# Performance work log

Measured on AMD Instinct MI355X. Metric: run time of the kernel, lower is better.

## Reference

```python
import jax, jax.numpy as jnp
import numpy as np
import math

EMBED = 512
DIM2 = 768

def setup_inputs() -> dict:
    key = jax.random.key(0)
    ks = jax.random.split(key, 14)
    B, L1, L2 = 16, 2048, 1024
    s1 = 1.0 / math.sqrt(EMBED)
    s2 = 1.0 / math.sqrt(DIM2)
    inp = {
        'input_tensor1': jax.random.normal(ks[0], (B, EMBED, L1), jnp.float32),
        'input_tensor2': jax.random.normal(ks[1], (B, DIM2, L2), jnp.float32),
        # Linear params for modality 1 (512 -> 512)
        'Wq1': jax.random.normal(ks[2], (EMBED, EMBED), jnp.float32) * s1,
        'bq1': jnp.zeros((EMBED,), jnp.float32),
        'Wk1': jax.random.normal(ks[3], (EMBED, EMBED), jnp.float32) * s1,
        'bk1': jnp.zeros((EMBED,), jnp.float32),
        'Wv1': jax.random.normal(ks[4], (EMBED, EMBED), jnp.float32) * s1,
        'bv1': jnp.zeros((EMBED,), jnp.float32),
        # Linear params for modality 2 (768 -> 512)
        'Wq2': jax.random.normal(ks[5], (DIM2, EMBED), jnp.float32) * s2,
        'bq2': jnp.zeros((EMBED,), jnp.float32),
        'Wk2': jax.random.normal(ks[6], (DIM2, EMBED), jnp.float32) * s2,
        'bk2': jnp.zeros((EMBED,), jnp.float32),
        'Wv2': jax.random.normal(ks[7], (DIM2, EMBED), jnp.float32) * s2,
        'bv2': jnp.zeros((EMBED,), jnp.float32),
    }
    return inp


def reference(input_tensor1, input_tensor2,
              Wq1, bq1, Wk1, bk1, Wv1, bv1,
              Wq2, bq2, Wk2, bk2, Wv2, bv2):
    scale = 1.0 / math.sqrt(EMBED)
    # [B, C, L] -> [B, L, C]
    x1 = jnp.swapaxes(input_tensor1, 1, 2)  # [B, L1, 512]
    x2 = jnp.swapaxes(input_tensor2, 1, 2)  # [B, L2, 768]
    q1 = x1 @ Wq1 + bq1  # [B, L1, E]
    k1 = x1 @ Wk1 + bk1
    v1 = x1 @ Wv1 + bv1
    q2 = x2 @ Wq2 + bq2  # [B, L2, E]
    k2 = x2 @ Wk2 + bk2
    v2 = x2 @ Wv2 + bv2
    # direction 1: queries from modality 2 attend to modality 1
    scores1 = jnp.einsum('bif,bjf->bij', q2, k1) * scale  # [B, L2, L1]
    probs1 = jax.nn.sigmoid(scores1)
    ctx1 = jnp.einsum('bij,bjf->bif', probs1, v1)  # [B, L2, E]
    # direction 2: queries from modality 1 attend to modality 2
    scores2 = jnp.einsum('bif,bjf->bij', q1, k2) * scale  # [B, L1, L2]
    probs2 = jax.nn.sigmoid(scores2)
    ctx2 = jnp.einsum('bij,bjf->bif', probs2, v2)  # [B, L1, E]
    return (ctx2, probs2, ctx1, probs1)
```

## Files before the change

### kernel.cpp

```cpp
#include <hip/hip_runtime.h>
#include <hip/hip_bf16.h>

#define DEVFN __device__ __forceinline__

typedef __attribute__((ext_vector_type(4))) float f32x4;
typedef __attribute__((ext_vector_type(8))) short s16x8;
typedef __attribute__((ext_vector_type(2))) short s16x2;
typedef __attribute__((ext_vector_type(8))) __bf16 bf16x8;

union FragU { s16x8 s; bf16x8 b; };

DEVFN short f2bs(float x) {
  union { __hip_bfloat16 h; short s; } u;
  u.h = __float2bfloat16(x);
  return u.s;
}

DEVFN void gload16(const void* g, void* l) {
  __builtin_amdgcn_global_load_lds(
      (const __attribute__((address_space(1))) void*)g,
      (__attribute__((address_space(3))) void*)l, 16, 0, 0);
}

template <int N> DEVFN void waitcnt_vm() {
  if constexpr (N == 0) asm volatile("s_waitcnt vmcnt(0)" ::: "memory");
  else if constexpr (N == 3) asm volatile("s_waitcnt vmcnt(3)" ::: "memory");
  else if constexpr (N == 4) asm volatile("s_waitcnt vmcnt(4)" ::: "memory");
  else if constexpr (N == 6) asm volatile("s_waitcnt vmcnt(6)" ::: "memory");
  else if constexpr (N == 8) asm volatile("s_waitcnt vmcnt(8)" ::: "memory");
  else static_assert(N == 0, "unsupported vmcnt");
}

__global__ __launch_bounds__(256) void transpose_cvt(
    const float* __restrict__ in, short* __restrict__ out, int C, int L) {
  __shared__ float tile[64][33];
  const int l0 = blockIdx.x * 32, c0 = blockIdx.y * 64;
  const size_t base = (size_t)blockIdx.z * C * L;
  const int tx = threadIdx.x, ty = threadIdx.y;
#pragma unroll
  for (int i = ty; i < 64; i += 8)
    tile[i][tx] = in[base + (size_t)(c0 + i) * L + l0 + tx];
  __syncthreads();
#pragma unroll
  for (int i = ty; i < 32; i += 8) {
    s16x2 v;
    v[0] = f2bs(tile[2 * tx][i]);
    v[1] = f2bs(tile[2 * tx + 1][i]);
    *(s16x2*)&out[base + (size_t)(l0 + i) * C + c0 + 2 * tx] = v;
  }
}

__global__ __launch_bounds__(256) void prep_weights(
    const float* __restrict__ Wq1, const float* __restrict__ Wk1,
    const float* __restrict__ Wv1, const float* __restrict__ Wq2,
    const float* __restrict__ Wk2, const float* __restrict__ Wv2,
    short* wq1t, short* wk1t, short* wv1t,
    short* wq2t, short* wk2t, short* wv2t,
    const float* __restrict__ bq1, const float* __restrict__ bk1,
    const float* __restrict__ bq2, const float* __restrict__ bk2,
    float* b1c, float* b2c) {
  const int z = blockIdx.z;
  if (z == 6) {
    if (blockIdx.y != 0 || blockIdx.x >= 8) return;
    const int bx = blockIdx.x;
    const int tid = threadIdx.y * 32 + threadIdx.x;
    const int i = (bx & 3) * 256 + tid;
    const float* s = (bx < 4) ? ((i < 512) ? bq1 : bk1)
                              : ((i < 512) ? bq2 : bk2);
    float* d = (bx < 4) ? b1c : b2c;
    d[i] = s[i & 511];
    return;
  }
  const float* W; short* O; int C;
  switch (z) {
    case 0: W = Wq1; O = wq1t; C = 512; break;
    case 1: W = Wk1; O = wk1t; C = 512; break;
    case 2: W = Wv1; O = wv1t; C = 512; break;
    case 3: W = Wq2; O = wq2t; C = 768; break;
    case 4: W = Wk2; O = wk2t; C = 768; break;
    default: W = Wv2; O = wv2t; C = 768; break;
  }
  if (blockIdx.y * 64 >= (unsigned)C) return;
  const int L = 512;
  __shared__ float tile[64][33];
  const int l0 = blockIdx.x * 32, c0 = blockIdx.y * 64;
  const int tx = threadIdx.x, ty = threadIdx.y;
#pragma unroll
  for (int i = ty; i < 64; i += 8)
    tile[i][tx] = W[(size_t)(c0 + i) * L + l0 + tx];
  __syncthreads();
#pragma unroll
  for (int i = ty; i < 32; i += 8) {
    s16x2 v;
    v[0] = f2bs(tile[2 * tx][i]);
    v[1] = f2bs(tile[2 * tx + 1][i]);
    *(s16x2*)&O[(size_t)(l0 + i) * C + c0 + 2 * tx] = v;
  }
}

template <int OUTMODE, int BIASMODE, int MR>
__global__ __launch_bounds__(512, 2) void gemm8(
    const short* __restrict__ Ap, const short* __restrict__ Btp,
    const float* __restrict__ bias, void* __restrict__ Cptr,
    short* __restrict__ C2p,
    int K, int lda, int ldb, int ldc,
    long long sA, long long sB, long long sC, float scale) {
  constexpr int BM = MR * 32;
  constexpr int BN = 256;
  constexpr int LA = BM / 128;
  constexpr int LB = BN / 128;
  constexpr int LPT = LA + LB;
  constexpr int ABYTES = BM * 64;
  constexpr int BUFB = (BM + BN) * 64;
  constexpr int MH = MR / 2;
  __shared__ __align__(16) char smem[4 * BUFB];
  const int tid = threadIdx.x;
  const int lane = tid & 63, wid = tid >> 6;
  const int wm = wid >> 2, wn = wid & 3;

  const unsigned gx = gridDim.x, gy = gridDim.y, gz = gridDim.z;
  const unsigned NB = gx * gy * gz;
  unsigned h = blockIdx.x + gx * (blockIdx.y + gy * blockIdx.z);
  unsigned l = ((NB & 7u) == 0u) ? (h & 7u) * (NB >> 3) + (h >> 3) : h;
  const unsigned bx = l % gx;
  const unsigned rem = l / gx;
  const unsigned by = rem % gy;
  const unsigned bz = rem / gy;

  const int zb = bz;
  const int m0 = by * BM, n0 = bx * BN;
  const char* Ab = (const char*)(Ap + (size_t)zb * sA);
  const char* Bb = (const char*)(Btp + (size_t)zb * sB);
  const size_t lda2 = (size_t)lda * 2, ldb2 = (size_t)ldb * 2;

  int s_r[2], s_cb[2];
#pragma unroll
  for (int j = 0; j < 2; ++j) {
    const int d = j * 8192 + tid * 16;
    const int line = d >> 7;
    s_r[j] = line * 2 + ((d >> 6) & 1);
    s_cb[j] = (d & 63) ^ ((line & 3) << 4);
  }

  f32x4 acc[MR][4] = {};
  const int frow = lane & 15, fkg = lane >> 4;

  int ra[MR], rb[4];
#pragma unroll
  for (int mf = 0; mf < MR; ++mf) {
    const int R = wm * (MR * 16) + mf * 16 + frow;
    ra[mf] = (R >> 1) * 128 + (R & 1) * 64 + ((fkg * 16) ^ (((R >> 1) & 3) << 4));
  }
#pragma unroll
  for (int nf = 0; nf < 4; ++nf) {
    const int R = wn * 64 + nf * 16 + frow;
    rb[nf] = (R >> 1) * 128 + (R & 1) * 64 + ((fkg * 16) ^ (((R >> 1) & 3) << 4));
  }

  const int NT = K >> 5;

#define STAGE_A(t)                                                       \
  {                                                                      \
    char* base_ = smem + ((t) & 3) * BUFB;                               \
    const size_t kb_ = (size_t)(t) * 64;                                 \
    _Pragma("unroll")                                                    \
    for (int j = 0; j < LA; ++j)                                         \
      gload16(Ab + (size_t)(m0 + s_r[j]) * lda2 + kb_ + s_cb[j],         \
              base_ + j * 8192 + tid * 16);                              \
  }
#define STAGE_B(t)                                                       \
  {                                                                      \
    char* base_ = smem + ((t) & 3) * BUFB + ABYTES;                      \
    const size_t kb_ = (size_t)(t) * 64;                                 \
    _Pragma("unroll")                                                    \
    for (int j = 0; j < LB; ++j)                                         \
      gload16(Bb + (size_t)(n0 + s_r[j]) * ldb2 + kb_ + s_cb[j],         \
              base_ + j * 8192 + tid * 16);                              \
  }

  STAGE_A(0); STAGE_B(0);
  STAGE_A(1); STAGE_B(1);
  STAGE_A(2); STAGE_B(2);
  waitcnt_vm<2 * LPT>();
  __builtin_amdgcn_sched_barrier(0);
  __builtin_amdgcn_s_barrier();
  __builtin_amdgcn_sched_barrier(0);

  for (int t = 0; t < NT; ++t) {
    const char* la = smem + (t & 3) * BUFB;
    const char* lb = la + ABYTES;
    FragU fa[MR], fb[4];
    if (t + 3 < NT) STAGE_A(t + 3);
#pragma unroll
    for (int mf = 0; mf < MH; ++mf) fa[mf].s = *(const s16x8*)(la + ra[mf]);
#pragma unroll
    for (int nf = 0; nf < 4; ++nf) fb[nf].s = *(const s16x8*)(lb + rb[nf]);
    __builtin_amdgcn_s_barrier();
    asm volatile("s_waitcnt lgkmcnt(0)" ::: "memory");
    __builtin_amdgcn_sched_barrier(0);
    __builtin_amdgcn_s_setprio(1);
#pragma unroll
    for (int mf = 0; mf < MH; ++mf)
#pragma unroll
      for (int nf = 0; nf < 4; ++nf)
        acc[mf][nf] = __builtin_amdgcn_mfma_f32_16x16x32_bf16(
            fa[mf].b, fb[nf].b, acc[mf][nf], 0, 0, 0);
    __builtin_amdgcn_s_setprio(0);
    __builtin_amdgcn_s_barrier();
    if (t + 3 < NT) STAGE_B(t + 3);
#pragma unroll
    for (int mf = MH; mf < MR; ++mf) fa[mf].s = *(const s16x8*)(la + ra[mf]);
    __builtin_amdgcn_s_barrier();
    asm volatile("s_waitcnt lgkmcnt(0)" ::: "memory");
    __builtin_amdgcn_sched_barrier(0);
    __builtin_amdgcn_s_setprio(1);
#pragma unroll
    for (int mf = MH; mf < MR; ++mf)
#pragma unroll
      for (int nf = 0; nf < 4; ++nf)
        acc[mf][nf] = __builtin_amdgcn_mfma_f32_16x16x32_bf16(
            fa[mf].b, fb[nf].b, acc[mf][nf], 0, 0, 0);
    __builtin_amdgcn_s_setprio(0);
    if (t + 3 < NT) {
      waitcnt_vm<2 * LPT>();
    } else if (t + 2 < NT) {
      waitcnt_vm<LPT>();
    } else if (t + 1 < NT) {
      waitcnt_vm<0>();
    } else {
      break;
    }
    __builtin_amdgcn_sched_barrier(0);
    __builtin_amdgcn_s_barrier();
    __builtin_amdgcn_sched_barrier(0);
  }
#undef STAGE_A
#undef STAGE_B

  const int rbase = (lane >> 4) * 4, cbase = lane & 15;
#pragma unroll
  for (int mf = 0; mf < MR; ++mf) {
#pragma unroll
    for (int nf = 0; nf < 4; ++nf) {
      const int gcol = n0 + wn * 64 + nf * 16 + cbase;
      float bn = (BIASMODE == 1) ? bias[gcol] : 0.f;
#pragma unroll
      for (int r = 0; r < 4; ++r) {
        const int grow = m0 + wm * (MR * 16) + mf * 16 + rbase + r;
        const size_t idx = (size_t)zb * sC + (size_t)grow * ldc + gcol;
        float v = acc[mf][nf][r];
        if constexpr (BIASMODE == 2) v += bias[grow]; else v += bn;
        if constexpr (OUTMODE == 0) {
          ((short*)Cptr)[idx] = f2bs(v);
        } else if constexpr (OUTMODE == 1) {
          ((float*)Cptr)[idx] = v;
        } else if constexpr (OUTMODE == 2) {
          ((float*)Cptr)[idx] = 1.0f / (1.0f + __expf(-v * scale));
        } else {
          float p = 1.0f / (1.0f + __expf(-v * scale));
          ((float*)Cptr)[idx] = p;
          C2p[idx] = f2bs(p);
        }
      }
    }
  }
}

template <int OUTMODE, int BIASMODE, int AF32>
__global__ __launch_bounds__(256) void gemm_bt(
    const void* __restrict__ Aptr, const short* __restrict__ Btp,
    const float* __restrict__ bias, void* __restrict__ Cptr,
    short* __restrict__ C2p,
    int K, int lda, int ldb, int ldc,
    long long sA, long long sB, long long sC, float scale) {
  __shared__ __align__(16) short lsA[128 * 64];
  __shared__ __align__(16) short lsB[128 * 64];
  const int tid = threadIdx.x;
  const int lane = tid & 63, wid = tid >> 6;
  const int zb = blockIdx.z;
  const int m0 = blockIdx.y * 128, n0 = blockIdx.x * 128;
  const short* Ab = AF32 ? nullptr : (const short*)Aptr + (size_t)zb * sA;
  const float* Af = AF32 ? (const float*)Aptr + (size_t)zb * sA : nullptr;
  const short* Bt = Btp + (size_t)zb * sB;

  f32x4 acc[4][4] = {};
  const int woffM = (wid >> 1) * 64, woffN = (wid & 1) * 64;
  const int frow = lane & 15, fkg = lane >> 4;

  for (int k0 = 0; k0 < K; k0 += 64) {
    if (k0) __syncthreads();
    if constexpr (!AF32) {
#pragma unroll
      for (int i = 0; i < 4; ++i) {
        const int f = i * 4096 + tid * 16;
        const int row = f >> 7, colb = f & 127;
        gload16((const char*)Ab + ((size_t)(m0 + row) * lda + k0) * 2 + colb,
                (char*)lsA + f);
      }
    } else {
#pragma unroll
      for (int i = 0; i < 8; ++i) {
        int f = tid + i * 256;
        int row = f >> 4, c4 = f & 15;
        f32x4 v = *(const f32x4*)&Af[(size_t)(m0 + row) * lda + k0 + c4 * 4];
        union { short s[4]; unsigned long long q; } cv;
#pragma unroll
        for (int j = 0; j < 4; ++j) cv.s[j] = f2bs(v[j]);
        *(unsigned long long*)&lsA[row * 64 + c4 * 4] = cv.q;
      }
    }
#pragma unroll
    for (int i = 0; i < 4; ++i) {
      const int f = i * 4096 + tid * 16;
      const int row = f >> 7, colb = f & 127;
      gload16((const char*)Bt + ((size_t)(n0 + row) * ldb + k0) * 2 + colb,
              (char*)lsB + f);
    }
    __syncthreads();
#pragma unroll
    for (int kk = 0; kk < 2; ++kk) {
      const int kb = kk * 32 + fkg * 8;
      FragU fa[4], fb[4];
#pragma unroll
      for (int mf = 0; mf < 4; ++mf)
        fa[mf].s = *(const s16x8*)&lsA[(woffM + mf * 16 + frow) * 64 + kb];
#pragma unroll
      for (int nf = 0; nf < 4; ++nf)
        fb[nf].s = *(const s16x8*)&lsB[(woffN + nf * 16 + frow) * 64 + kb];
#pragma unroll
      for (int mf = 0; mf < 4; ++mf)
#pragma unroll
        for (int nf = 0; nf < 4; ++nf)
          acc[mf][nf] = __builtin_amdgcn_mfma_f32_16x16x32_bf16(
              fa[mf].b, fb[nf].b, acc[mf][nf], 0, 0, 0);
    }
  }

  const int rbase = (lane >> 4) * 4, cbase = lane & 15;
#pragma unroll
  for (int mf = 0; mf < 4; ++mf) {
#pragma unroll
    for (int nf = 0; nf < 4; ++nf) {
      const int gcol = n0 + woffN + nf * 16 + cbase;
      float bn = (BIASMODE == 1) ? bias[gcol] : 0.f;
#pragma unroll
      for (int r = 0; r < 4; ++r) {
        const int grow = m0 + woffM + mf * 16 + rbase + r;
        const size_t idx = (size_t)zb * sC + (size_t)grow * ldc + gcol;
        float v = acc[mf][nf][r];
        if constexpr (BIASMODE == 2) v += bias[grow]; else v += bn;
        if constexpr (OUTMODE == 0) {
          ((short*)Cptr)[idx] = f2bs(v);
        } else if constexpr (OUTMODE == 1) {
          ((float*)Cptr)[idx] = v;
        } else if constexpr (OUTMODE == 2) {
          ((float*)Cptr)[idx] = 1.0f / (1.0f + __expf(-v * scale));
        } else {
          float p = 1.0f / (1.0f + __expf(-v * scale));
          ((float*)Cptr)[idx] = p;
          C2p[idx] = f2bs(p);
        }
      }
    }
  }
}

extern "C" void kernel_launch(void* const* d_in, const int* in_sizes, int n_in,
                              void* d_out, int out_size, void* d_ws, size_t ws_size,
                              hipStream_t stream) {
  const float* in1 = (const float*)d_in[0];
  const float* in2 = (const float*)d_in[1];
  const float* Wq1 = (const float*)d_in[2];  const float* bq1 = (const float*)d_in[3];
  const float* Wk1 = (const float*)d_in[4];  const float* bk1 = (const float*)d_in[5];
  const float* Wv1 = (const float*)d_in[6];  const float* bv1 = (const float*)d_in[7];
  const float* Wq2 = (const float*)d_in[8];  const float* bq2 = (const float*)d_in[9];
  const float* Wk2 = (const float*)d_in[10]; const float* bk2 = (const float*)d_in[11];
  const float* Wv2 = (const float*)d_in[12]; const float* bv2 = (const float*)d_in[13];

  float* out = (float*)d_out;
  float* ctx2   = out;
  float* probs2 = out + (size_t)16 * 2048 * 512;
  float* ctx1   = probs2 + (size_t)16 * 2048 * 1024;
  float* probs1 = ctx1 + (size_t)16 * 1024 * 512;

  char* ws = (char*)d_ws;
  constexpr size_t O_WQ1T = 0;
  constexpr size_t O_WK1T = O_WQ1T + (size_t)512 * 512 * 2;
  constexpr size_t O_WV1T = O_WK1T + (size_t)512 * 512 * 2;
  constexpr size_t O_WQ2T = O_WV1T + (size_t)512 * 512 * 2;
  constexpr size_t O_WK2T = O_WQ2T + (size_t)768 * 512 * 2;
  constexpr size_t O_WV2T = O_WK2T + (size_t)768 * 512 * 2;
  constexpr size_t O_B1   = O_WV2T + (size_t)768 * 512 * 2;
  constexpr size_t O_B2   = O_B1 + 4096;
  constexpr size_t O_QK1  = O_B2 + 4096;
  constexpr size_t O_V1T  = O_QK1 + (size_t)32768 * 1024 * 2;
  constexpr size_t O_QK2  = O_V1T + (size_t)16 * 512 * 2048 * 2;
  constexpr size_t O_V2T  = O_QK2 + (size_t)16384 * 1024 * 2;
  constexpr size_t O_X1B  = O_V2T + (size_t)16 * 512 * 1024 * 2;
  constexpr size_t O_X2B  = O_X1B + (size_t)32768 * 512 * 2;
  constexpr size_t O_PB1  = O_X2B + (size_t)16384 * 768 * 2;
  constexpr size_t O_PB2  = O_PB1 + (size_t)16 * 1024 * 2048 * 2;
  constexpr size_t NEED_A = O_PB2 + (size_t)16 * 2048 * 1024 * 2;
  constexpr size_t NEED_B = O_PB1;

  short* wq1t = (short*)(ws + O_WQ1T);
  short* wk1t = (short*)(ws + O_WK1T);
  short* wv1t = (short*)(ws + O_WV1T);
  short* wq2t = (short*)(ws + O_WQ2T);
  short* wk2t = (short*)(ws + O_WK2T);
  short* wv2t = (short*)(ws + O_WV2T);
  float* b1c  = (float*)(ws + O_B1);
  float* b2c  = (float*)(ws + O_B2);
  short* qk1  = (short*)(ws + O_QK1);
  short* v1t  = (short*)(ws + O_V1T);
  short* qk2  = (short*)(ws + O_QK2);
  short* v2t  = (short*)(ws + O_V2T);
  short* x1b  = (short*)(ws + O_X1B);
  short* x2b  = (short*)(ws + O_X2B);
  short* pb1  = (short*)(ws + O_PB1);
  short* pb2  = (short*)(ws + O_PB2);

  const bool tierA = ws_size >= NEED_A;
  const bool tierB = ws_size >= NEED_B;
  if (!tierB) { x1b = (short*)probs1; x2b = (short*)probs2; }

  dim3 blk256(256), blk512(512);
  dim3 blkT(32, 8);

  transpose_cvt<<<dim3(64, 8, 16), blkT, 0, stream>>>(in1, x1b, 512, 2048);
  transpose_cvt<<<dim3(32, 12, 16), blkT, 0, stream>>>(in2, x2b, 768, 1024);
  prep_weights<<<dim3(16, 12, 7), blkT, 0, stream>>>(
      Wq1, Wk1, Wv1, Wq2, Wk2, Wv2, wq1t, wk1t, wv1t, wq2t, wk2t, wv2t,
      bq1, bk1, bq2, bk2, b1c, b2c);

  const float scale = 0.04419417382415922f;
  const short* q1p = qk1;
  const short* k1p = qk1 + 512;
  const short* q2p = qk2;
  const short* k2p = qk2 + 512;

  if (tierA) {
    gemm8<0, 1, 8><<<dim3(4, 128, 1), blk512, 0, stream>>>(
        x1b, wq1t, b1c, qk1, nullptr, 512, 512, 512, 1024, 0, 0, 0, 1.f);
    gemm8<0, 1, 8><<<dim3(4, 64, 1), blk512, 0, stream>>>(
        x2b, wq2t, b2c, qk2, nullptr, 768, 768, 768, 1024, 0, 0, 0, 1.f);
    gemm8<0, 2, 8><<<dim3(8, 2, 16), blk512, 0, stream>>>(
        wv1t, x1b, bv1, v1t, nullptr, 512, 512, 512, 2048,
        0, (long long)2048 * 512, (long long)512 * 2048, 1.f);
    gemm8<0, 2, 4><<<dim3(4, 4, 16), blk512, 0, stream>>>(
        wv2t, x2b, bv2, v2t, nullptr, 768, 768, 768, 1024,
        0, (long long)1024 * 768, (long long)512 * 1024, 1.f);
    gemm8<3, 0, 8><<<dim3(8, 4, 16), blk512, 0, stream>>>(
        q2p, k1p, nullptr, probs1, pb1, 512, 1024, 1024, 2048,
        (long long)1024 * 1024, (long long)2048 * 1024, (long long)1024 * 2048, scale);
    gemm8<3, 0, 8><<<dim3(4, 8, 16), blk512, 0, stream>>>(
        q1p, k2p, nullptr, probs2, pb2, 512, 1024, 1024, 1024,
        (long long)2048 * 1024, (long long)1024 * 1024, (long long)2048 * 1024, scale);
    gemm8<1, 0, 4><<<dim3(2, 8, 16), blk512, 0, stream>>>(
        pb1, v1t, nullptr, ctx1, nullptr, 2048, 2048, 2048, 512,
        (long long)1024 * 2048, (long long)512 * 2048, (long long)1024 * 512, 1.f);
    gemm8<1, 0, 8><<<dim3(2, 8, 16), blk512, 0, stream>>>(
        pb2, v2t, nullptr, ctx2, nullptr, 1024, 1024, 1024, 512,
        (long long)2048 * 1024, (long long)512 * 1024, (long long)2048 * 512, 1.f);
  } else {
    gemm_bt<0, 1, 0><<<dim3(8, 256, 1), blk256, 0, stream>>>(
        x1b, wq1t, b1c, qk1, nullptr, 512, 512, 512, 1024, 0, 0, 0, 1.f);
    gemm_bt<0, 1, 0><<<dim3(8, 128, 1), blk256, 0, stream>>>(
        x2b, wq2t, b2c, qk2, nullptr, 768, 768, 768, 1024, 0, 0, 0, 1.f);
    gemm_bt<0, 2, 0><<<dim3(16, 4, 16), blk256, 0, stream>>>(
        wv1t, x1b, bv1, v1t, nullptr, 512, 512, 512, 2048,
        0, (long long)2048 * 512, (long long)512 * 2048, 1.f);
    gemm_bt<0, 2, 0><<<dim3(8, 4, 16), blk256, 0, stream>>>(
        wv2t, x2b, bv2, v2t, nullptr, 768, 768, 768, 1024,
        0, (long long)1024 * 768, (long long)512 * 1024, 1.f);
    gemm_bt<2, 0, 0><<<dim3(16, 8, 16), blk256, 0, stream>>>(
        q2p, k1p, nullptr, probs1, nullptr, 512, 1024, 1024, 2048,
        (long long)1024 * 1024, (long long)2048 * 1024, (long long)1024 * 2048, scale);
    gemm_bt<2, 0, 0><<<dim3(8, 16, 16), blk256, 0, stream>>>(
        q1p, k2p, nullptr, probs2, nullptr, 512, 1024, 1024, 1024,
        (long long)2048 * 1024, (long long)1024 * 1024, (long long)2048 * 1024, scale);
    gemm_bt<1, 0, 1><<<dim3(4, 8, 16), blk256, 0, stream>>>(
        probs1, v1t, nullptr, ctx1, nullptr, 2048, 2048, 2048, 512,
        (long long)1024 * 2048, (long long)512 * 2048, (long long)1024 * 512, 1.f);
    gemm_bt<1, 0, 1><<<dim3(4, 16, 16), blk256, 0, stream>>>(
        probs2, v2t, nullptr, ctx2, nullptr, 1024, 1024, 1024, 512,
        (long long)2048 * 1024, (long long)512 * 1024, (long long)2048 * 512, 1.f);
  }
}
```

Baseline: 458.7 us.

## Replace 8-wave 256-wide GEMM with 4-wave 128-wide triple-buffered kernel

Swaps the 512-thread GEMM (BN=256, 4-stage buffer, split A/B staging with two MFMA phases per k-step) for a 256-thread kernel with BN=128. It uses 3 LDS buffers with a prefetch depth of 2 and a single fused stage/compute phase per k-step. Each wave still computes MW×4 fragments. Grids double in the N dimension. The aim is smaller LDS per block and fewer barriers, at the cost of less B reuse per block and a shallower prefetch pipeline, which may expose memory latency.

```diff
diff --git a/kernel.cpp b/kernel.cpp
--- a/kernel.cpp
+++ b/kernel.cpp
@@ -24,7 +24,6 @@
 
 template <int N> DEVFN void waitcnt_vm() {
   if constexpr (N == 0) asm volatile("s_waitcnt vmcnt(0)" ::: "memory");
-  else if constexpr (N == 3) asm volatile("s_waitcnt vmcnt(3)" ::: "memory");
   else if constexpr (N == 4) asm volatile("s_waitcnt vmcnt(4)" ::: "memory");
   else if constexpr (N == 6) asm volatile("s_waitcnt vmcnt(6)" ::: "memory");
   else if constexpr (N == 8) asm volatile("s_waitcnt vmcnt(8)" ::: "memory");
@@ -98,25 +97,23 @@
   }
 }
 
-template <int OUTMODE, int BIASMODE, int MR>
-__global__ __launch_bounds__(512, 2) void gemm8(
+template <int OUTMODE, int BIASMODE, int MW>
+__global__ __launch_bounds__(256, 2) void gemm4(
     const short* __restrict__ Ap, const short* __restrict__ Btp,
     const float* __restrict__ bias, void* __restrict__ Cptr,
     short* __restrict__ C2p,
     int K, int lda, int ldb, int ldc,
     long long sA, long long sB, long long sC, float scale) {
-  constexpr int BM = MR * 32;
-  constexpr int BN = 256;
-  constexpr int LA = BM / 128;
-  constexpr int LB = BN / 128;
+  constexpr int BM = MW * 32;
+  constexpr int LA = BM / 64;
+  constexpr int LB = 2;
   constexpr int LPT = LA + LB;
   constexpr int ABYTES = BM * 64;
-  constexpr int BUFB = (BM + BN) * 64;
-  constexpr int MH = MR / 2;
-  __shared__ __align__(16) char smem[4 * BUFB];
+  constexpr int BUFB = (BM + 128) * 64;
+  __shared__ __align__(16) char smem[3 * BUFB];
   const int tid = threadIdx.x;
   const int lane = tid & 63, wid = tid >> 6;
-  const int wm = wid >> 2, wn = wid & 3;
+  const int wm = wid >> 1, wn = wid & 1;
 
   const unsigned gx = gridDim.x, gy = gridDim.y, gz = gridDim.z;
   const unsigned NB = gx * gy * gz;
@@ -128,27 +125,27 @@
   const unsigned bz = rem / gy;
 
   const int zb = bz;
-  const int m0 = by * BM, n0 = bx * BN;
+  const int m0 = by * BM, n0 = bx * 128;
   const char* Ab = (const char*)(Ap + (size_t)zb * sA);
   const char* Bb = (const char*)(Btp + (size_t)zb * sB);
   const size_t lda2 = (size_t)lda * 2, ldb2 = (size_t)ldb * 2;
 
-  int s_r[2], s_cb[2];
-#pragma unroll
-  for (int j = 0; j < 2; ++j) {
-    const int d = j * 8192 + tid * 16;
+  int s_r[LA], s_cb[LA];
+#pragma unroll
+  for (int j = 0; j < LA; ++j) {
+    const int d = j * 4096 + tid * 16;
     const int line = d >> 7;
     s_r[j] = line * 2 + ((d >> 6) & 1);
     s_cb[j] = (d & 63) ^ ((line & 3) << 4);
   }
 
-  f32x4 acc[MR][4] = {};
+  f32x4 acc[MW][4] = {};
   const int frow = lane & 15, fkg = lane >> 4;
 
-  int ra[MR], rb[4];
-#pragma unroll
-  for (int mf = 0; mf < MR; ++mf) {
-    const int R = wm * (MR * 16) + mf * 16 + frow;
+  int ra[MW], rb[4];
+#pragma unroll
+  for (int mf = 0; mf < MW; ++mf) {
+    const int R = wm * (MW * 16) + mf * 16 + frow;
     ra[mf] = (R >> 1) * 128 + (R & 1) * 64 + ((fkg * 16) ^ (((R >> 1) & 3) << 4));
   }
 #pragma unroll
@@ -159,71 +156,47 @@
 
   const int NT = K >> 5;
 
-#define STAGE_A(t)                                                       \
+#define STAGE(t)                                                         \
   {                                                                      \
-    char* base_ = smem + ((t) & 3) * BUFB;                               \
+    char* base_ = smem + ((t) % 3) * BUFB;                               \
     const size_t kb_ = (size_t)(t) * 64;                                 \
     _Pragma("unroll")                                                    \
     for (int j = 0; j < LA; ++j)                                         \
       gload16(Ab + (size_t)(m0 + s_r[j]) * lda2 + kb_ + s_cb[j],         \
-              base_ + j * 8192 + tid * 16);                              \
-  }
-#define STAGE_B(t)                                                       \
-  {                                                                      \
-    char* base_ = smem + ((t) & 3) * BUFB + ABYTES;                      \
-    const size_t kb_ = (size_t)(t) * 64;                                 \
+              base_ + j * 4096 + tid * 16);                              \
     _Pragma("unroll")                                                    \
     for (int j = 0; j < LB; ++j)                                         \
       gload16(Bb + (size_t)(n0 + s_r[j]) * ldb2 + kb_ + s_cb[j],         \
-              base_ + j * 8192 + tid * 16);                              \
-  }
-
-  STAGE_A(0); STAGE_B(0);
-  STAGE_A(1); STAGE_B(1);
-  STAGE_A(2); STAGE_B(2);
-  waitcnt_vm<2 * LPT>();
+              base_ + ABYTES + j * 4096 + tid * 16);                     \
+  }
+
+  STAGE(0);
+  STAGE(1);
+  waitcnt_vm<LPT>();
   __builtin_amdgcn_sched_barrier(0);
   __builtin_amdgcn_s_barrier();
   __builtin_amdgcn_sched_barrier(0);
 
   for (int t = 0; t < NT; ++t) {
-    const char* la = smem + (t & 3) * BUFB;
+    if (t + 2 < NT) STAGE(t + 2);
+    const char* la = smem + (t % 3) * BUFB;
     const char* lb = la + ABYTES;
-    FragU fa[MR], fb[4];
-    if (t + 3 < NT) STAGE_A(t + 3);
-#pragma unroll
-    for (int mf = 0; mf < MH; ++mf) fa[mf].s = *(const s16x8*)(la + ra[mf]);
+    FragU fa[MW], fb[4];
+#pragma unroll
+    for (int mf = 0; mf < MW; ++mf) fa[mf].s = *(const s16x8*)(la + ra[mf]);
 #pragma unroll
     for (int nf = 0; nf < 4; ++nf) fb[nf].s = *(const s16x8*)(lb + rb[nf]);
-    __builtin_amdgcn_s_barrier();
     asm volatile("s_waitcnt lgkmcnt(0)" ::: "memory");
     __builtin_amdgcn_sched_barrier(0);
     __builtin_amdgcn_s_setprio(1);
 #pragma unroll
-    for (int mf = 0; mf < MH; ++mf)
+    for (int mf = 0; mf < MW; ++mf)
 #pragma unroll
       for (int nf = 0; nf < 4; ++nf)
         acc[mf][nf] = __builtin_amdgcn_mfma_f32_16x16x32_bf16(
             fa[mf].b, fb[nf].b, acc[mf][nf], 0, 0, 0);
     __builtin_amdgcn_s_setprio(0);
-    __builtin_amdgcn_s_barrier();
-    if (t + 3 < NT) STAGE_B(t + 3);
-#pragma unroll
-    for (int mf = MH; mf < MR; ++mf) fa[mf].s = *(const s16x8*)(la + ra[mf]);
-    __builtin_amdgcn_s_barrier();
-    asm volatile("s_waitcnt lgkmcnt(0)" ::: "memory");
-    __builtin_amdgcn_sched_barrier(0);
-    __builtin_amdgcn_s_setprio(1);
-#pragma unroll
-    for (int mf = MH; mf < MR; ++mf)
-#pragma unroll
-      for (int nf = 0; nf < 4; ++nf)
-        acc[mf][nf] = __builtin_amdgcn_mfma_f32_16x16x32_bf16(
-            fa[mf].b, fb[nf].b, acc[mf][nf], 0, 0, 0);
-    __builtin_amdgcn_s_setprio(0);
-    if (t + 3 < NT) {
-      waitcnt_vm<2 * LPT>();
-    } else if (t + 2 < NT) {
+    if (t + 2 < NT) {
       waitcnt_vm<LPT>();
     } else if (t + 1 < NT) {
       waitcnt_vm<0>();
@@ -234,19 +207,18 @@
     __builtin_amdgcn_s_barrier();
     __builtin_amdgcn_sched_barrier(0);
   }
-#undef STAGE_A
-#undef STAGE_B
+#undef STAGE
 
   const int rbase = (lane >> 4) * 4, cbase = lane & 15;
 #pragma unroll
-  for (int mf = 0; mf < MR; ++mf) {
+  for (int mf = 0; mf < MW; ++mf) {
 #pragma unroll
     for (int nf = 0; nf < 4; ++nf) {
       const int gcol = n0 + wn * 64 + nf * 16 + cbase;
       float bn = (BIASMODE == 1) ? bias[gcol] : 0.f;
 #pragma unroll
       for (int r = 0; r < 4; ++r) {
-        const int grow = m0 + wm * (MR * 16) + mf * 16 + rbase + r;
+        const int grow = m0 + wm * (MW * 16) + mf * 16 + rbase + r;
         const size_t idx = (size_t)zb * sC + (size_t)grow * ldc + gcol;
         float v = acc[mf][nf][r];
         if constexpr (BIASMODE == 2) v += bias[grow]; else v += bn;
@@ -424,7 +396,7 @@
   const bool tierB = ws_size >= NEED_B;
   if (!tierB) { x1b = (short*)probs1; x2b = (short*)probs2; }
 
-  dim3 blk256(256), blk512(512);
+  dim3 blk256(256);
   dim3 blkT(32, 8);
 
   transpose_cvt<<<dim3(64, 8, 16), blkT, 0, stream>>>(in1, x1b, 512, 2048);
@@ -440,26 +412,26 @@
   const short* k2p = qk2 + 512;
 
   if (tierA) {
-    gemm8<0, 1, 8><<<dim3(4, 128, 1), blk512, 0, stream>>>(
+    gemm4<0, 1, 8><<<dim3(8, 128, 1), blk256, 0, stream>>>(
         x1b, wq1t, b1c, qk1, nullptr, 512, 512, 512, 1024, 0, 0, 0, 1.f);
-    gemm8<0, 1, 8><<<dim3(4, 64, 1), blk512, 0, stream>>>(
+    gemm4<0, 1, 8><<<dim3(8, 64, 1), blk256, 0, stream>>>(
         x2b, wq2t, b2c, qk2, nullptr, 768, 768, 768, 1024, 0, 0, 0, 1.f);
-    gemm8<0, 2, 8><<<dim3(8, 2, 16), blk512, 0, stream>>>(
+    gemm4<0, 2, 8><<<dim3(16, 2, 16), blk256, 0, stream>>>(
         wv1t, x1b, bv1, v1t, nullptr, 512, 512, 512, 2048,
         0, (long long)2048 * 512, (long long)512 * 2048, 1.f);
-    gemm8<0, 2, 4><<<dim3(4, 4, 16), blk512, 0, stream>>>(
+    gemm4<0, 2, 4><<<dim3(8, 4, 16), blk256, 0, stream>>>(
         wv2t, x2b, bv2, v2t, nullptr, 768, 768, 768, 1024,
         0, (long long)1024 * 768, (long long)512 * 1024, 1.f);
-    gemm8<3, 0, 8><<<dim3(8, 4, 16), blk512, 0, stream>>>(
+    gemm4<3, 0, 8><<<dim3(16, 4, 16), blk256, 0, stream>>>(
         q2p, k1p, nullptr, probs1, pb1, 512, 1024, 1024, 2048,
         (long long)1024 * 1024, (long long)2048 * 1024, (long long)1024 * 2048, scale);
-    gemm8<3, 0, 8><<<dim3(4, 8, 16), blk512, 0, stream>>>(
+    gemm4<3, 0, 8><<<dim3(8, 8, 16), blk256, 0, stream>>>(
         q1p, k2p, nullptr, probs2, pb2, 512, 1024, 1024, 1024,
         (long long)2048 * 1024, (long long)1024 * 1024, (long long)2048 * 1024, scale);
-    gemm8<1, 0, 4><<<dim3(2, 8, 16), blk512, 0, stream>>>(
+    gemm4<1, 0, 4><<<dim3(4, 8, 16), blk256, 0, stream>>>(
         pb1, v1t, nullptr, ctx1, nullptr, 2048, 2048, 2048, 512,
         (long long)1024 * 2048, (long long)512 * 2048, (long long)1024 * 512, 1.f);
-    gemm8<1, 0, 8><<<dim3(2, 8, 16), blk512, 0, stream>>>(
+    gemm4<1, 0, 8><<<dim3(4, 8, 16), blk256, 0, stream>>>(
         pb2, v2t, nullptr, ctx2, nullptr, 1024, 1024, 1024, 512,
         (long long)2048 * 1024, (long long)512 * 1024, (long long)2048 * 512, 1.f);
   } else {
```

New measurement: 474.9 us. +3.5%, slower.

## Merge paired GEMM launches into dual-problem kernels and use nontemporal fp32 stores

Applied to the files above, without the earlier changes.

The gemm8 kernel becomes gemm8d, which takes two independent GEMM problems and splits a flat 1D grid between them by block index. The QK, V, score/sigmoid and context GEMM pairs each run as one launch. This cuts launch count and lets the two problems share the GPU instead of each leaving a partially filled tail wave. The fp32 output stores (probs and ctx) now use nontemporal hints so they do not pollute cache. The V2/ctx2 halves are forced to share one MR tile size, which changes their tiling and could cost some efficiency.

```diff
diff --git a/kernel.cpp b/kernel.cpp
--- a/kernel.cpp
+++ b/kernel.cpp
@@ -99,12 +99,20 @@
 }
 
 template <int OUTMODE, int BIASMODE, int MR>
-__global__ __launch_bounds__(512, 2) void gemm8(
-    const short* __restrict__ Ap, const short* __restrict__ Btp,
-    const float* __restrict__ bias, void* __restrict__ Cptr,
-    short* __restrict__ C2p,
-    int K, int lda, int ldb, int ldc,
-    long long sA, long long sB, long long sC, float scale) {
+__global__ __launch_bounds__(512, 2) void gemm8d(
+    const short* __restrict__ A0, const short* __restrict__ B0,
+    const float* __restrict__ bias0, void* __restrict__ C0,
+    short* __restrict__ D0,
+    int K0, int lda0, int ldb0, int ldc0,
+    long long sA0, long long sB0, long long sC0,
+    unsigned gx0, unsigned gy0, unsigned nb0,
+    const short* __restrict__ A1, const short* __restrict__ B1,
+    const float* __restrict__ bias1, void* __restrict__ C1,
+    short* __restrict__ D1,
+    int K1, int lda1, int ldb1, int ldc1,
+    long long sA1, long long sB1, long long sC1,
+    unsigned gx1, unsigned gy1,
+    float scale) {
   constexpr int BM = MR * 32;
   constexpr int BN = 256;
   constexpr int LA = BM / 128;
@@ -118,10 +126,26 @@
   const int lane = tid & 63, wid = tid >> 6;
   const int wm = wid >> 2, wn = wid & 3;
 
-  const unsigned gx = gridDim.x, gy = gridDim.y, gz = gridDim.z;
-  const unsigned NB = gx * gy * gz;
-  unsigned h = blockIdx.x + gx * (blockIdx.y + gy * blockIdx.z);
-  unsigned l = ((NB & 7u) == 0u) ? (h & 7u) * (NB >> 3) + (h >> 3) : h;
+  const unsigned h = blockIdx.x;
+  const bool sec = h >= nb0;
+  const unsigned hh = sec ? h - nb0 : h;
+  const unsigned nb = sec ? gridDim.x - nb0 : nb0;
+  const unsigned gx = sec ? gx1 : gx0;
+  const unsigned gy = sec ? gy1 : gy0;
+  const short* Ap = sec ? A1 : A0;
+  const short* Btp = sec ? B1 : B0;
+  const float* bias = sec ? bias1 : bias0;
+  void* Cptr = sec ? C1 : C0;
+  short* C2p = sec ? D1 : D0;
+  const int K = sec ? K1 : K0;
+  const int lda = sec ? lda1 : lda0;
+  const int ldb = sec ? ldb1 : ldb0;
+  const int ldc = sec ? ldc1 : ldc0;
+  const long long sA = sec ? sA1 : sA0;
+  const long long sB = sec ? sB1 : sB0;
+  const long long sC = sec ? sC1 : sC0;
+
+  unsigned l = ((nb & 7u) == 0u) ? (hh & 7u) * (nb >> 3) + (hh >> 3) : hh;
   const unsigned bx = l % gx;
   const unsigned rem = l / gx;
   const unsigned by = rem % gy;
@@ -253,12 +277,13 @@
         if constexpr (OUTMODE == 0) {
           ((short*)Cptr)[idx] = f2bs(v);
         } else if constexpr (OUTMODE == 1) {
-          ((float*)Cptr)[idx] = v;
+          __builtin_nontemporal_store(v, &((float*)Cptr)[idx]);
         } else if constexpr (OUTMODE == 2) {
-          ((float*)Cptr)[idx] = 1.0f / (1.0f + __expf(-v * scale));
+          float p = 1.0f / (1.0f + __expf(-v * scale));
+          __builtin_nontemporal_store(p, &((float*)Cptr)[idx]);
         } else {
           float p = 1.0f / (1.0f + __expf(-v * scale));
-          ((float*)Cptr)[idx] = p;
+          __builtin_nontemporal_store(p, &((float*)Cptr)[idx]);
           C2p[idx] = f2bs(p);
         }
       }
@@ -440,28 +465,32 @@
   const short* k2p = qk2 + 512;
 
   if (tierA) {
-    gemm8<0, 1, 8><<<dim3(4, 128, 1), blk512, 0, stream>>>(
-        x1b, wq1t, b1c, qk1, nullptr, 512, 512, 512, 1024, 0, 0, 0, 1.f);
-    gemm8<0, 1, 8><<<dim3(4, 64, 1), blk512, 0, stream>>>(
-        x2b, wq2t, b2c, qk2, nullptr, 768, 768, 768, 1024, 0, 0, 0, 1.f);
-    gemm8<0, 2, 8><<<dim3(8, 2, 16), blk512, 0, stream>>>(
+    gemm8d<0, 1, 8><<<dim3(768), blk512, 0, stream>>>(
+        x1b, wq1t, b1c, qk1, nullptr, 512, 512, 512, 1024, 0, 0, 0,
+        4u, 128u, 512u,
+        x2b, wq2t, b2c, qk2, nullptr, 768, 768, 768, 1024, 0, 0, 0,
+        4u, 64u, 1.f);
+    gemm8d<0, 2, 4><<<dim3(768), blk512, 0, stream>>>(
         wv1t, x1b, bv1, v1t, nullptr, 512, 512, 512, 2048,
-        0, (long long)2048 * 512, (long long)512 * 2048, 1.f);
-    gemm8<0, 2, 4><<<dim3(4, 4, 16), blk512, 0, stream>>>(
+        0, (long long)2048 * 512, (long long)512 * 2048,
+        8u, 4u, 512u,
         wv2t, x2b, bv2, v2t, nullptr, 768, 768, 768, 1024,
-        0, (long long)1024 * 768, (long long)512 * 1024, 1.f);
-    gemm8<3, 0, 8><<<dim3(8, 4, 16), blk512, 0, stream>>>(
+        0, (long long)1024 * 768, (long long)512 * 1024,
+        4u, 4u, 1.f);
+    gemm8d<3, 0, 8><<<dim3(1024), blk512, 0, stream>>>(
         q2p, k1p, nullptr, probs1, pb1, 512, 1024, 1024, 2048,
-        (long long)1024 * 1024, (long long)2048 * 1024, (long long)1024 * 2048, scale);
-    gemm8<3, 0, 8><<<dim3(4, 8, 16), blk512, 0, stream>>>(
+        (long long)1024 * 1024, (long long)2048 * 1024, (long long)1024 * 2048,
+        8u, 4u, 512u,
         q1p, k2p, nullptr, probs2, pb2, 512, 1024, 1024, 1024,
-        (long long)2048 * 1024, (long long)1024 * 1024, (long long)2048 * 1024, scale);
-    gemm8<1, 0, 4><<<dim3(2, 8, 16), blk512, 0, stream>>>(
+        (long long)2048 * 1024, (long long)1024 * 1024, (long long)2048 * 1024,
+        4u, 8u, scale);
+    gemm8d<1, 0, 4><<<dim3(768), blk512, 0, stream>>>(
         pb1, v1t, nullptr, ctx1, nullptr, 2048, 2048, 2048, 512,
-        (long long)1024 * 2048, (long long)512 * 2048, (long long)1024 * 512, 1.f);
-    gemm8<1, 0, 8><<<dim3(2, 8, 16), blk512, 0, stream>>>(
+        (long long)1024 * 2048, (long long)512 * 2048, (long long)1024 * 512,
+        2u, 8u, 256u,
         pb2, v2t, nullptr, ctx2, nullptr, 1024, 1024, 1024, 512,
-        (long long)2048 * 1024, (long long)512 * 1024, (long long)2048 * 512, 1.f);
+        (long long)2048 * 1024, (long long)512 * 1024, (long long)2048 * 512,
+        2u, 16u, 1.f);
   } else {
     gemm_bt<0, 1, 0><<<dim3(8, 256, 1), blk256, 0, stream>>>(
         x1b, wq1t, b1c, qk1, nullptr, 512, 512, 512, 1024, 0, 0, 0, 1.f);
```

New measurement: 440.3 us. -4.0%, faster.
